# Kernel optimization log

Measured on AMD Instinct MI355X. Metric: run time of the kernel, lower is better.

Reference implementation:

```python
import jax, jax.numpy as jnp
import numpy as np

B, SEQ, DIM = 2, 2048, 1024
HEADS, DIM_HEAD = 16, 64
INNER = HEADS * DIM_HEAD
SCALE = DIM_HEAD ** -0.5


def rotate_half(x):
    # pair consecutive dims (d r) with r=2: (x1, x2) -> (-x2, x1)
    xp = x.reshape(*x.shape[:-1], -1, 2)
    x1, x2 = xp[..., 0], xp[..., 1]
    return jnp.stack((-x2, x1), axis=-1).reshape(x.shape)


def apply_rotary_emb(freqs, t):
    # freqs: [n, rot_dim] angles; t: [b, h, n, d]
    rot_dim = freqs.shape[-1]
    t_rot, t_pass = t[..., :rot_dim], t[..., rot_dim:]
    t_rot = t_rot * jnp.cos(freqs) + rotate_half(t_rot) * jnp.sin(freqs)
    return jnp.concatenate([t_rot, t_pass], axis=-1)


def setup_inputs() -> dict:
    key = jax.random.key(0)
    ks = jax.random.split(key, 4)
    x = jax.random.normal(ks[0], (B, SEQ, DIM), dtype=jnp.float32)
    mask = jnp.ones((B, SEQ), dtype=bool)
    rotary_pos_emb = jax.random.uniform(ks[1], (SEQ, DIM_HEAD), dtype=jnp.float32)
    Wqkv = jax.random.normal(ks[2], (DIM, 3 * INNER), dtype=jnp.float32) * 0.02
    Wout = jax.random.normal(ks[3], (INNER, DIM), dtype=jnp.float32) * 0.02
    bout = jnp.zeros((DIM,), dtype=jnp.float32)
    return {"x": x, "mask": mask, "rotary_pos_emb": rotary_pos_emb,
            "Wqkv": Wqkv, "Wout": Wout, "bout": bout}


def reference(x, mask, rotary_pos_emb, Wqkv, Wout, bout):
    b, n, _ = x.shape
    qkv = x @ Wqkv                                   # [b, n, 3*inner]
    q, k, v = jnp.split(qkv, 3, axis=-1)

    def to_heads(t):
        return t.reshape(b, n, HEADS, DIM_HEAD).transpose(0, 2, 1, 3)  # [b,h,n,d]

    q, k, v = to_heads(q), to_heads(k), to_heads(v)
    freqs = rotary_pos_emb[:n, :]
    # NB: original applies rotary to q, k AND v
    q = apply_rotary_emb(freqs, q)
    k = apply_rotary_emb(freqs, k)
    v = apply_rotary_emb(freqs, v)
    q = q * SCALE

    dots = jnp.einsum('bhid,bhjd->bhij', q, k)       # [b,h,n,n]
    mask_value = -jnp.finfo(dots.dtype).max
    pad = mask[:, None, None, :]                     # [b,1,1,n] keep where True
    dots = jnp.where(pad, dots, mask_value)
    idx = jnp.arange(n)
    causal = idx[None, :] > idx[:, None]             # j >= i + (j-i+1) with i==j==n
    dots = jnp.where(causal[None, None], mask_value, dots)

    attn = jax.nn.softmax(dots, axis=-1)
    out = jnp.einsum('bhij,bhjd->bhid', attn, v)     # [b,h,n,d]
    out = out.transpose(0, 2, 1, 3).reshape(b, n, INNER)
    return out @ Wout + bout
```

## Files before the change

### kernel.cpp

```cpp
#include <hip/hip_runtime.h>
#include <hip/hip_bf16.h>
#include <stdint.h>

#define DEVI __device__ __forceinline__

typedef __bf16 bf16x8 __attribute__((ext_vector_type(8)));
typedef float f32x4 __attribute__((ext_vector_type(4)));
typedef float f32x16 __attribute__((ext_vector_type(16)));

static constexpr int SEQ = 2048;
static constexpr int DIM = 1024;
static constexpr int HEADS = 16;
static constexpr int NQKV = 3072;
static constexpr int MROWS = 4096;
static constexpr float QSCALE = 0.125f;
static constexpr float LOG2E = 1.4426950408889634f;

DEVI unsigned short f2bf(float f) {
  unsigned int u = __builtin_bit_cast(unsigned int, f);
  u += 0x7FFFu + ((u >> 16) & 1u);
  return (unsigned short)(u >> 16);
}

DEVI bf16x8 ld8(const unsigned short* p) {
  return __builtin_bit_cast(bf16x8, *(const uint4*)p);
}

DEVI f32x4 mfma16(bf16x8 a, bf16x8 b, f32x4 c) {
  return __builtin_amdgcn_mfma_f32_16x16x32_bf16(a, b, c, 0, 0, 0);
}

DEVI f32x16 mfma32(bf16x8 a, bf16x8 b, f32x16 c) {
  return __builtin_amdgcn_mfma_f32_32x32x16_bf16(a, b, c, 0, 0, 0);
}

DEVI void load_lds16(const void* g, void* l) {
  __builtin_amdgcn_global_load_lds((const __attribute__((address_space(1))) void*)g,
                                   (__attribute__((address_space(3))) void*)l,
                                   16, 0, 0);
}

DEVI int swz(int row, int kelem) {
  return row * 64 + (kelem ^ ((row & 7) << 3));
}

DEVI unsigned cvtpk(float lo, float hi) {
  unsigned r;
  asm("v_cvt_pk_bf16_f32 %0, %1, %2" : "=v"(r) : "v"(lo), "v"(hi));
  return r;
}

DEVI void pl32swap(unsigned& a, unsigned& b) {
  asm volatile("v_permlane32_swap_b32 %0, %1" : "+v"(a), "+v"(b));
}
DEVI float xhalf_max(float v) { return fmaxf(v, __shfl_xor(v, 32)); }
DEVI float xhalf_sum(float v) { return v + __shfl_xor(v, 32); }

DEVI void transpose_tile(const float* __restrict__ in, unsigned short* __restrict__ out,
                         int Kd, int Nd, int bx, int by, int tid,
                         unsigned short (*T)[68]) {
  const int n0 = bx * 64, k0 = by * 64;
  const int rr = tid >> 4, cc = (tid & 15) * 4;
#pragma unroll
  for (int p = 0; p < 4; ++p) {
    const int r = p * 16 + rr;
    float4 f = *(const float4*)(in + (size_t)(k0 + r) * Nd + n0 + cc);
    T[r][cc + 0] = f2bf(f.x);
    T[r][cc + 1] = f2bf(f.y);
    T[r][cc + 2] = f2bf(f.z);
    T[r][cc + 3] = f2bf(f.w);
  }
  __syncthreads();
#pragma unroll
  for (int p = 0; p < 4; ++p) {
    const int rn = p * 16 + rr;
    ushort4 v;
    v.x = T[cc + 0][rn];
    v.y = T[cc + 1][rn];
    v.z = T[cc + 2][rn];
    v.w = T[cc + 3][rn];
    *(ushort4*)(out + (size_t)(n0 + rn) * Kd + k0 + cc) = v;
  }
}

__global__ __launch_bounds__(256) void k_prep(
    const float* __restrict__ x, unsigned short* __restrict__ xb,
    const float* __restrict__ rope, float* __restrict__ cosb, float* __restrict__ sinb,
    const float* __restrict__ Wqkv, unsigned short* __restrict__ wqkvt,
    const float* __restrict__ Wout, unsigned short* __restrict__ woutt) {
  __shared__ unsigned short T[64][68];
  const int bid = blockIdx.x, tid = threadIdx.x;
  if (bid < 2048) {
    const size_t i = ((size_t)bid * 256 + tid) * 8;
    float4 f0 = *(const float4*)(x + i);
    float4 f1 = *(const float4*)(x + i + 4);
    ushort4 v0, v1;
    v0.x = f2bf(f0.x); v0.y = f2bf(f0.y); v0.z = f2bf(f0.z); v0.w = f2bf(f0.w);
    v1.x = f2bf(f1.x); v1.y = f2bf(f1.y); v1.z = f2bf(f1.z); v1.w = f2bf(f1.w);
    *(ushort4*)(xb + i) = v0;
    *(ushort4*)(xb + i + 4) = v1;
  } else if (bid < 2560) {
    const int i = (bid - 2048) * 256 + tid;
    float f = rope[i];
    cosb[i] = cosf(f);
    sinb[i] = sinf(f);
  } else if (bid < 3328) {
    const int idx = bid - 2560;
    transpose_tile(Wqkv, wqkvt, DIM, NQKV, idx % 48, idx / 48, tid, T);
  } else {
    const int idx = bid - 3328;
    transpose_tile(Wout, woutt, DIM, DIM, idx % 16, idx / 16, tid, T);
  }
}

__global__ __launch_bounds__(512, 1) void k_gemm_qkv(
    const unsigned short* __restrict__ xb, const unsigned short* __restrict__ wt,
    const float* __restrict__ cosb, const float* __restrict__ sinb,
    unsigned short* __restrict__ qb, unsigned short* __restrict__ kb,
    unsigned short* __restrict__ vb) {
  __shared__ __align__(16) unsigned short Ab[2][2][8192];
  __shared__ __align__(16) unsigned short Bb[2][12288];
  const int tid = threadIdx.x, lane = tid & 63, wid = tid >> 6;
  const int wm = wid >> 2, wn = wid & 3;
  const int m0 = blockIdx.x * 256, n0 = blockIdx.y * 192;
  const int la15 = lane & 15, l16 = lane >> 4;
  const int pS0 = tid, pS1 = tid + 512;
  const int sr0 = pS0 >> 3, sr1 = pS1 >> 3;
  const int sc0 = ((pS0 & 7) ^ (sr0 & 7)) * 8, sc1 = ((pS1 & 7) ^ (sr1 & 7)) * 8;
  const int bsr = tid >> 3;
  const int bsc = ((tid & 7) ^ (bsr & 7)) * 8;

  auto stageA = [&](int h, int s) {
    const unsigned short* src = xb + (size_t)(m0 + h * 128) * DIM + s * 64;
    unsigned short* dst = &Ab[s & 1][h][0];
    load_lds16(src + (size_t)sr0 * DIM + sc0, dst + pS0 * 8);
    load_lds16(src + (size_t)sr1 * DIM + sc1, dst + pS1 * 8);
  };
  auto stageB3 = [&](int t, int s) {
    const unsigned short* src = wt + (size_t)(n0 + t * 64 + bsr) * DIM + s * 64;
    load_lds16(src + bsc, &Bb[s & 1][t * 4096] + tid * 8);
  };

  f32x4 acc[8][3] = {};
  stageA(0, 0); stageA(1, 0); stageB3(0, 0); stageB3(1, 0); stageB3(2, 0);
  stageA(0, 1); stageA(1, 1); stageB3(0, 1); stageB3(1, 1); stageB3(2, 1);

#pragma unroll 1
  for (int s = 0; s < 16; ++s) {
    const unsigned short* Ah = &Ab[s & 1][wm][0];
    const unsigned short* Bh = &Bb[s & 1][0];
    const int rb = wn * 48;
    bf16x8 bfr[3][2];
#pragma unroll
    for (int q = 0; q < 4; ++q) {
      if (q == 0) {
        if (s == 0)       asm volatile("s_waitcnt vmcnt(7)" ::: "memory");
        else if (s == 15) asm volatile("s_waitcnt vmcnt(0)" ::: "memory");
        else              asm volatile("s_waitcnt vmcnt(3)" ::: "memory");
        __syncthreads();
      }
      if (q == 2) __syncthreads();
      bf16x8 afr[2][2];
      if (q == 0) {
#pragma unroll
        for (int ni = 0; ni < 3; ++ni)
#pragma unroll
          for (int kk = 0; kk < 2; ++kk)
            bfr[ni][kk] = ld8(&Bh[swz(rb + ni * 16 + la15, kk * 32 + 8 * l16)]);
      }
#pragma unroll
      for (int mi = 0; mi < 2; ++mi)
#pragma unroll
        for (int kk = 0; kk < 2; ++kk)
          afr[mi][kk] = ld8(&Ah[swz(q * 32 + mi * 16 + la15, kk * 32 + 8 * l16)]);
      if (q == 0)      { if (s >= 1 && s + 1 < 16) stageA(0, s + 1); }
      else if (q == 1) { if (s >= 1 && s + 1 < 16) stageA(1, s + 1); }
      else if (q == 2) { if (s + 2 < 16) stageB3(0, s + 2); }
      else             { if (s + 2 < 16) { stageB3(1, s + 2); stageB3(2, s + 2); } }
      asm volatile("s_waitcnt lgkmcnt(0)" ::: "memory");
      __builtin_amdgcn_sched_barrier(0);
      __builtin_amdgcn_s_setprio(1);
#pragma unroll
      for (int kk = 0; kk < 2; ++kk)
#pragma unroll
        for (int mi = 0; mi < 2; ++mi)
#pragma unroll
          for (int ni = 0; ni < 3; ++ni)
            acc[2 * q + mi][ni] = mfma16(afr[mi][kk], bfr[ni][kk], acc[2 * q + mi][ni]);
      __builtin_amdgcn_s_setprio(0);
    }
  }

#pragma unroll
  for (int mq = 0; mq < 8; ++mq) {
#pragma unroll
    for (int ni = 0; ni < 3; ++ni) {
      const int ng = n0 + wn * 48 + ni * 16 + la15;
      const int d = ng & 63;
      const int part = ng >> 10;
      const int h = (ng & 1023) >> 6;
      const int mg0 = m0 + wm * 128 + mq * 16 + 4 * l16;
      const int s0 = mg0 & (SEQ - 1), b = mg0 >> 11;
      const size_t bh = (size_t)(b * HEADS + h);
      if (part == 2) {
        ushort4 vv;
#pragma unroll
        for (int r = 0; r < 4; ++r) {
          const int s = s0 + r;
          float v = acc[mq][ni][r];
          float p = __shfl_xor(v, 1);
          float cv = cosb[(s << 6) + d], sv = sinb[(s << 6) + d];
          float rot = v * cv + ((d & 1) ? p : -p) * sv;
          ((unsigned short*)&vv)[r] = f2bf(rot);
        }
        *(ushort4*)(vb + (bh * 64 + d) * SEQ + s0) = vv;
      } else {
#pragma unroll
        for (int r = 0; r < 4; ++r) {
          const int s = s0 + r;
          float v = acc[mq][ni][r];
          float p = __shfl_xor(v, 1);
          float cv = cosb[(s << 6) + d], sv = sinb[(s << 6) + d];
          float rot = v * cv + ((d & 1) ? p : -p) * sv;
          if (part == 0) {
            qb[(bh * SEQ + s) * 64 + d] = f2bf(rot * (QSCALE * LOG2E));
          } else {
            kb[(bh * SEQ + s) * 64 + d] = f2bf(rot);
          }
        }
      }
    }
  }
}

__global__ __launch_bounds__(256) void k_flash(
    const unsigned short* __restrict__ qb, const unsigned short* __restrict__ kb,
    const unsigned short* __restrict__ vtb, unsigned short* __restrict__ ao) {
  __shared__ __align__(16) unsigned short Ks[2][2][4096];
  __shared__ __align__(16) unsigned short Vt[2][4096];
  const int bh = blockIdx.x;
  const int qt = 31 - blockIdx.y;
  const int tid = threadIdx.x, lane = tid & 63, wid = tid >> 6;
  const int wq = wid >> 1, wk = wid & 1;
  const int la31 = lane & 31, h = lane >> 5;
  const unsigned short* kbh = kb + (size_t)bh * SEQ * 64;
  const unsigned short* vbh = vtb + (size_t)bh * 64 * SEQ;
  const int b = bh >> 4, hh = bh & 15;
  const int sslot = ((lane & 7) ^ (lane >> 3)) * 8;
  float* mrg = (float*)&Ks[0][0][0];
  const int mbase = wq * 2176;

  auto stageK = [&](int buf, int t) {
    const int kv0 = t * 64;
#pragma unroll
    for (int i = 0; i < 4; ++i) {
      const int chunk = wq * 4 + i;
      const int row = chunk * 8 + (lane >> 3);
      load_lds16(kbh + ((size_t)(kv0 + row) << 6) + sslot, &Ks[buf][wk][chunk * 512]);
    }
  };
  auto stageV = [&](int t) {
    const int kv0 = t * 64;
#pragma unroll
    for (int i = 0; i < 4; ++i) {
      const int chunk = wq * 4 + i;
      const int row = chunk * 8 + (lane >> 3);
      load_lds16(vbh + (size_t)row * SEQ + kv0 + sslot, &Vt[wk][chunk * 512]);
    }
  };

  const int q0 = qt * 64 + wq * 32;
  const int qr = q0 + la31;
  const unsigned short* qp = qb + ((size_t)bh * SEQ + qr) * 64;
  bf16x8 qf0 = ld8(qp + 0 + 8 * h);
  bf16x8 qf1 = ld8(qp + 16 + 8 * h);
  bf16x8 qf2 = ld8(qp + 32 + 8 * h);
  bf16x8 qf3 = ld8(qp + 48 + 8 * h);

  f32x16 o0 = {}, o1 = {};
  float m = -1e30f, l = 0.f;
  const int nkv = qt + 1;
  const int nst = (nkv + 1) >> 1;

  if (wk < nkv) stageK(0, wk);
#pragma unroll 1
  for (int st = 0; st < nst; ++st) {
    const int cur = st & 1;
    const int t = 2 * st + wk;
    const bool live = (t < nkv);
    __syncthreads();
    if (live) stageV(t);
    { const int tn = 2 * (st + 1) + wk; if (tn < nkv) stageK(cur ^ 1, tn); }

    bf16x8 pa0, pa1, pa2, pa3;
    if (live) {
      const int kv0 = t * 64;
      const unsigned short* Kc = &Ks[cur][wk][0];
      f32x16 st0 = {}, st1 = {};
      __builtin_amdgcn_s_setprio(1);
#pragma unroll
      for (int ks = 0; ks < 4; ++ks) {
        bf16x8 qk = (ks == 0) ? qf0 : (ks == 1) ? qf1 : (ks == 2) ? qf2 : qf3;
        st0 = mfma32(ld8(&Kc[swz(la31, 16 * ks + 8 * h)]), qk, st0);
        st1 = mfma32(ld8(&Kc[swz(32 + la31, 16 * ks + 8 * h)]), qk, st1);
      }
      __builtin_amdgcn_s_setprio(0);
      if (kv0 + 63 > q0) {
#pragma unroll
        for (int r = 0; r < 16; ++r) {
          const int kvo = (r & 3) + 8 * (r >> 2) + 4 * h;
          st0[r] = (kv0 + kvo > qr) ? -1e30f : st0[r];
          st1[r] = (kv0 + 32 + kvo > qr) ? -1e30f : st1[r];
        }
      }
      float a8[8];
#pragma unroll
      for (int i = 0; i < 8; ++i)
        a8[i] = fmaxf(fmaxf(st0[i], st0[i + 8]), fmaxf(st1[i], st1[i + 8]));
      float a4_0 = fmaxf(a8[0], a8[4]), a4_1 = fmaxf(a8[1], a8[5]);
      float a4_2 = fmaxf(a8[2], a8[6]), a4_3 = fmaxf(a8[3], a8[7]);
      float pmax = fmaxf(fmaxf(a4_0, a4_1), fmaxf(a4_2, a4_3));
      const bool nor = __all(pmax <= m + 8.f);
      float scl = 1.f;
      if (!nor) {
        const float rowmax = xhalf_max(pmax);
        const float mnew = fmaxf(m, rowmax);
        scl = exp2f(m - mnew);
        m = mnew;
      }
#pragma unroll
      for (int r = 0; r < 16; ++r) {
        st0[r] = exp2f(st0[r] - m);
        st1[r] = exp2f(st1[r] - m);
      }
      float s8[8];
#pragma unroll
      for (int i = 0; i < 8; ++i)
        s8[i] = (st0[i] + st0[i + 8]) + (st1[i] + st1[i + 8]);
      float s4_0 = s8[0] + s8[4], s4_1 = s8[1] + s8[5];
      float s4_2 = s8[2] + s8[6], s4_3 = s8[3] + s8[7];
      float psum = (s4_0 + s4_1) + (s4_2 + s4_3);
      const float rowsum = xhalf_sum(psum);
      if (nor) {
        l += rowsum;
      } else {
        l = l * scl + rowsum;
#pragma unroll
        for (int r = 0; r < 16; ++r) { o0[r] *= scl; o1[r] *= scl; }
      }
      unsigned w0 = cvtpk(st0[0], st0[1]),   w1 = cvtpk(st0[2], st0[3]);
      unsigned w2 = cvtpk(st0[4], st0[5]),   w3 = cvtpk(st0[6], st0[7]);
      unsigned w4 = cvtpk(st0[8], st0[9]),   w5 = cvtpk(st0[10], st0[11]);
      unsigned w6 = cvtpk(st0[12], st0[13]), w7 = cvtpk(st0[14], st0[15]);
      pl32swap(w0, w2); pl32swap(w1, w3); pl32swap(w4, w6); pl32swap(w5, w7);
      pa0 = __builtin_bit_cast(bf16x8, (uint4){w0, w1, w2, w3});
      pa1 = __builtin_bit_cast(bf16x8, (uint4){w4, w5, w6, w7});
      unsigned x0 = cvtpk(st1[0], st1[1]),   x1 = cvtpk(st1[2], st1[3]);
      unsigned x2 = cvtpk(st1[4], st1[5]),   x3 = cvtpk(st1[6], st1[7]);
      unsigned x4 = cvtpk(st1[8], st1[9]),   x5 = cvtpk(st1[10], st1[11]);
      unsigned x6 = cvtpk(st1[12], st1[13]), x7 = cvtpk(st1[14], st1[15]);
      pl32swap(x0, x2); pl32swap(x1, x3); pl32swap(x4, x6); pl32swap(x5, x7);
      pa2 = __builtin_bit_cast(bf16x8, (uint4){x0, x1, x2, x3});
      pa3 = __builtin_bit_cast(bf16x8, (uint4){x4, x5, x6, x7});
    }
    __syncthreads();
    if (live) {
      const unsigned short* Vc = &Vt[wk][0];
      __builtin_amdgcn_s_setprio(1);
      o0 = mfma32(ld8(&Vc[swz(la31, 0 + 8 * h)]), pa0, o0);
      o0 = mfma32(ld8(&Vc[swz(la31, 16 + 8 * h)]), pa1, o0);
      o0 = mfma32(ld8(&Vc[swz(la31, 32 + 8 * h)]), pa2, o0);
      o0 = mfma32(ld8(&Vc[swz(la31, 48 + 8 * h)]), pa3, o0);
      o1 = mfma32(ld8(&Vc[swz(32 + la31, 0 + 8 * h)]), pa0, o1);
      o1 = mfma32(ld8(&Vc[swz(32 + la31, 16 + 8 * h)]), pa1, o1);
      o1 = mfma32(ld8(&Vc[swz(32 + la31, 32 + 8 * h)]), pa2, o1);
      o1 = mfma32(ld8(&Vc[swz(32 + la31, 48 + 8 * h)]), pa3, o1);
      __builtin_amdgcn_s_setprio(0);
    }
  }

  __syncthreads();
  if (wk == 1) {
#pragma unroll
    for (int s = 0; s < 8; ++s) {
      f32x4 c;
      if (s < 4) { c[0]=o0[4*s]; c[1]=o0[4*s+1]; c[2]=o0[4*s+2]; c[3]=o0[4*s+3]; }
      else       { c[0]=o1[4*(s-4)]; c[1]=o1[4*(s-4)+1]; c[2]=o1[4*(s-4)+2]; c[3]=o1[4*(s-4)+3]; }
      *(f32x4*)&mrg[mbase + lane * 32 + 4 * (s ^ (lane & 7))] = c;
    }
    mrg[mbase + 2048 + lane] = m;
    mrg[mbase + 2112 + lane] = l;
  }
  __syncthreads();
  if (wk == 0) {
    const float m1 = mrg[mbase + 2048 + lane];
    const float l1 = mrg[mbase + 2112 + lane];
    const float mM = fmaxf(m, m1);
    const float sc0 = exp2f(m - mM), sc1 = exp2f(m1 - mM);
    const float lt = l * sc0 + l1 * sc1;
    const float rl = __builtin_amdgcn_rcpf(lt);
    unsigned short* aor = ao + ((size_t)(b * SEQ + qr)) * 1024 + hh * 64;
#pragma unroll
    for (int s = 0; s < 8; ++s) {
      f32x4 c = *(const f32x4*)&mrg[mbase + lane * 32 + 4 * (s ^ (lane & 7))];
      float v0, v1, v2, v3;
      if (s < 4) {
        v0 = (o0[4*s]   * sc0 + c[0] * sc1) * rl;
        v1 = (o0[4*s+1] * sc0 + c[1] * sc1) * rl;
        v2 = (o0[4*s+2] * sc0 + c[2] * sc1) * rl;
        v3 = (o0[4*s+3] * sc0 + c[3] * sc1) * rl;
      } else {
        v0 = (o1[4*(s-4)]   * sc0 + c[0] * sc1) * rl;
        v1 = (o1[4*(s-4)+1] * sc0 + c[1] * sc1) * rl;
        v2 = (o1[4*(s-4)+2] * sc0 + c[2] * sc1) * rl;
        v3 = (o1[4*(s-4)+3] * sc0 + c[3] * sc1) * rl;
      }
      uint2 uv;
      uv.x = cvtpk(v0, v1);
      uv.y = cvtpk(v2, v3);
      *(uint2*)(aor + (s < 4 ? 8 * s : 32 + 8 * (s - 4)) + 4 * h) = uv;
    }
  }
}

__global__ __launch_bounds__(256) void k_gemm_out(
    const unsigned short* __restrict__ ao, const unsigned short* __restrict__ wt,
    const float* __restrict__ bout, float* __restrict__ out) {
  __shared__ __align__(16) unsigned short As[128 * 64];
  __shared__ __align__(16) unsigned short Bs[64 * 64];
  const int m0 = blockIdx.x * 128, n0 = blockIdx.y * 64;
  const int lane = threadIdx.x & 63, wid = threadIdx.x >> 6;
  const int rsub = lane >> 3;
  const int ksw = ((lane & 7) ^ rsub) * 8;
  f32x4 acc[2][4] = {};
  for (int kt = 0; kt < DIM; kt += 64) {
    __syncthreads();
#pragma unroll
    for (int i = 0; i < 4; ++i) {
      const int chunk = wid * 4 + i;
      const int row = chunk * 8 + rsub;
      load_lds16(ao + (size_t)(m0 + row) * DIM + kt + ksw, As + chunk * 512);
    }
#pragma unroll
    for (int i = 0; i < 2; ++i) {
      const int chunk = wid * 2 + i;
      const int row = chunk * 8 + rsub;
      load_lds16(wt + (size_t)(n0 + row) * DIM + kt + ksw, Bs + chunk * 512);
    }
    __syncthreads();
#pragma unroll
    for (int kk = 0; kk < 2; ++kk) {
      bf16x8 af[2], bfv[4];
#pragma unroll
      for (int mi = 0; mi < 2; ++mi)
        af[mi] = ld8(&As[swz(wid * 32 + mi * 16 + (lane & 15),
                             kk * 32 + 8 * (lane >> 4))]);
#pragma unroll
      for (int ni = 0; ni < 4; ++ni)
        bfv[ni] = ld8(&Bs[swz(ni * 16 + (lane & 15),
                              kk * 32 + 8 * (lane >> 4))]);
#pragma unroll
      for (int mi = 0; mi < 2; ++mi)
#pragma unroll
        for (int ni = 0; ni < 4; ++ni)
          acc[mi][ni] = mfma16(af[mi], bfv[ni], acc[mi][ni]);
    }
  }
#pragma unroll
  for (int mi = 0; mi < 2; ++mi) {
#pragma unroll
    for (int ni = 0; ni < 4; ++ni) {
      const int ng = n0 + ni * 16 + (lane & 15);
      const float bn = bout[ng];
#pragma unroll
      for (int r = 0; r < 4; ++r) {
        const int mg = m0 + wid * 32 + mi * 16 + 4 * (lane >> 4) + r;
        out[(size_t)mg * DIM + ng] = acc[mi][ni][r] + bn;
      }
    }
  }
}

extern "C" void kernel_launch(void* const* d_in, const int* in_sizes, int n_in,
                              void* d_out, int out_size, void* d_ws, size_t ws_size,
                              hipStream_t stream) {
  const float* x    = (const float*)d_in[0];
  const float* rope = (const float*)d_in[2];
  const float* Wqkv = (const float*)d_in[3];
  const float* Wout = (const float*)d_in[4];
  const float* bout = (const float*)d_in[5];
  float* out = (float*)d_out;

  char* ws = (char*)d_ws;
  unsigned short* xb    = (unsigned short*)(ws + 0);
  unsigned short* wqkvt = (unsigned short*)(ws + 8388608);
  unsigned short* woutt = (unsigned short*)(ws + 14680064);
  float*          cosb  = (float*)(ws + 16777216);
  float*          sinb  = (float*)(ws + 17301504);
  unsigned short* qbuf  = (unsigned short*)(ws + 17825792);
  unsigned short* kbuf  = (unsigned short*)(ws + 26214400);
  unsigned short* vbuf  = (unsigned short*)(ws + 34603008);
  unsigned short* aob   = (unsigned short*)(ws + 42991616);

  k_prep<<<3584, 256, 0, stream>>>(x, xb, rope, cosb, sinb, Wqkv, wqkvt, Wout, woutt);
  k_gemm_qkv<<<dim3(16, 16), 512, 0, stream>>>(xb, wqkvt, cosb, sinb,
                                               qbuf, kbuf, vbuf);
  k_flash<<<dim3(32, 32), 256, 0, stream>>>(qbuf, kbuf, vbuf, aob);
  k_gemm_out<<<dim3(32, 16), 256, 0, stream>>>(aob, woutt, bout, out);
}
```

Before: 114.9 us.

## Pair causal query tiles per block and split KV across four waves

The flash kernel now launches half as many blocks with 512 threads. Each block processes two query tiles (31-j and j) so causal work is balanced across blocks. KV is split into 32-row sub-tiles spread over four waves per query group, with a two-stage tree merge of the partial softmax states through LDS. This targets tail imbalance and raises per-block parallelism, at the cost of extra barriers and merge traffic.

```diff
diff --git a/kernel.cpp b/kernel.cpp
--- a/kernel.cpp
+++ b/kernel.cpp
@@ -233,193 +233,216 @@
   }
 }
 
-__global__ __launch_bounds__(256) void k_flash(
+__global__ __launch_bounds__(512, 4) void k_flash(
     const unsigned short* __restrict__ qb, const unsigned short* __restrict__ kb,
     const unsigned short* __restrict__ vtb, unsigned short* __restrict__ ao) {
-  __shared__ __align__(16) unsigned short Ks[2][2][4096];
-  __shared__ __align__(16) unsigned short Vt[2][4096];
+  __shared__ __align__(16) unsigned short LDS[24576];
+  unsigned short (*Ks)[4][2048] = (unsigned short (*)[4][2048])&LDS[0];
+  unsigned short (*Vt)[2048] = (unsigned short (*)[2048])&LDS[16384];
+  float* scr = (float*)&LDS[0];
   const int bh = blockIdx.x;
-  const int qt = 31 - blockIdx.y;
+  const int j = blockIdx.y;
   const int tid = threadIdx.x, lane = tid & 63, wid = tid >> 6;
-  const int wq = wid >> 1, wk = wid & 1;
+  const int wq = wid >> 2, wk = wid & 3;
   const int la31 = lane & 31, h = lane >> 5;
   const unsigned short* kbh = kb + (size_t)bh * SEQ * 64;
   const unsigned short* vbh = vtb + (size_t)bh * 64 * SEQ;
   const int b = bh >> 4, hh = bh & 15;
-  const int sslot = ((lane & 7) ^ (lane >> 3)) * 8;
-  float* mrg = (float*)&Ks[0][0][0];
-  const int mbase = wq * 2176;
+
+  const int pA = wq * 128 + lane, pB = pA + 64;
+  const int rA = pA >> 3, rB = pB >> 3;
+  const int cA = (pA & 7) ^ (rA & 7), cB = (pB & 7) ^ (rB & 7);
+  const int kconA = rA * 64 + cA * 8, kconB = rB * 64 + cB * 8;
+  const int vconA = (2 * rA + (cA >> 2)) * SEQ + (cA & 3) * 8;
+  const int vconB = (2 * rB + (cB >> 2)) * SEQ + (cB & 3) * 8;
 
   auto stageK = [&](int buf, int t) {
-    const int kv0 = t * 64;
-#pragma unroll
-    for (int i = 0; i < 4; ++i) {
-      const int chunk = wq * 4 + i;
-      const int row = chunk * 8 + (lane >> 3);
-      load_lds16(kbh + ((size_t)(kv0 + row) << 6) + sslot, &Ks[buf][wk][chunk * 512]);
-    }
+    const size_t kv0 = (size_t)t * 32;
+    unsigned short* Kd = &Ks[buf][wk][0];
+    load_lds16(kbh + kv0 * 64 + kconA, Kd + pA * 8);
+    load_lds16(kbh + kv0 * 64 + kconB, Kd + pB * 8);
   };
   auto stageV = [&](int t) {
-    const int kv0 = t * 64;
-#pragma unroll
-    for (int i = 0; i < 4; ++i) {
-      const int chunk = wq * 4 + i;
-      const int row = chunk * 8 + (lane >> 3);
-      load_lds16(vbh + (size_t)row * SEQ + kv0 + sslot, &Vt[wk][chunk * 512]);
-    }
+    const size_t kv0 = (size_t)t * 32;
+    unsigned short* Vd = &Vt[wk][0];
+    load_lds16(vbh + kv0 + vconA, Vd + pA * 8);
+    load_lds16(vbh + kv0 + vconB, Vd + pB * 8);
   };
 
-  const int q0 = qt * 64 + wq * 32;
-  const int qr = q0 + la31;
-  const unsigned short* qp = qb + ((size_t)bh * SEQ + qr) * 64;
-  bf16x8 qf0 = ld8(qp + 0 + 8 * h);
-  bf16x8 qf1 = ld8(qp + 16 + 8 * h);
-  bf16x8 qf2 = ld8(qp + 32 + 8 * h);
-  bf16x8 qf3 = ld8(qp + 48 + 8 * h);
-
-  f32x16 o0 = {}, o1 = {};
-  float m = -1e30f, l = 0.f;
-  const int nkv = qt + 1;
-  const int nst = (nkv + 1) >> 1;
-
-  if (wk < nkv) stageK(0, wk);
 #pragma unroll 1
-  for (int st = 0; st < nst; ++st) {
-    const int cur = st & 1;
-    const int t = 2 * st + wk;
-    const bool live = (t < nkv);
-    __syncthreads();
-    if (live) stageV(t);
-    { const int tn = 2 * (st + 1) + wk; if (tn < nkv) stageK(cur ^ 1, tn); }
-
-    bf16x8 pa0, pa1, pa2, pa3;
-    if (live) {
-      const int kv0 = t * 64;
-      const unsigned short* Kc = &Ks[cur][wk][0];
-      f32x16 st0 = {}, st1 = {};
-      __builtin_amdgcn_s_setprio(1);
-#pragma unroll
-      for (int ks = 0; ks < 4; ++ks) {
-        bf16x8 qk = (ks == 0) ? qf0 : (ks == 1) ? qf1 : (ks == 2) ? qf2 : qf3;
-        st0 = mfma32(ld8(&Kc[swz(la31, 16 * ks + 8 * h)]), qk, st0);
-        st1 = mfma32(ld8(&Kc[swz(32 + la31, 16 * ks + 8 * h)]), qk, st1);
-      }
-      __builtin_amdgcn_s_setprio(0);
-      if (kv0 + 63 > q0) {
-#pragma unroll
-        for (int r = 0; r < 16; ++r) {
-          const int kvo = (r & 3) + 8 * (r >> 2) + 4 * h;
-          st0[r] = (kv0 + kvo > qr) ? -1e30f : st0[r];
-          st1[r] = (kv0 + 32 + kvo > qr) ? -1e30f : st1[r];
-        }
-      }
-      float a8[8];
-#pragma unroll
-      for (int i = 0; i < 8; ++i)
-        a8[i] = fmaxf(fmaxf(st0[i], st0[i + 8]), fmaxf(st1[i], st1[i + 8]));
-      float a4_0 = fmaxf(a8[0], a8[4]), a4_1 = fmaxf(a8[1], a8[5]);
-      float a4_2 = fmaxf(a8[2], a8[6]), a4_3 = fmaxf(a8[3], a8[7]);
-      float pmax = fmaxf(fmaxf(a4_0, a4_1), fmaxf(a4_2, a4_3));
-      const bool nor = __all(pmax <= m + 8.f);
-      float scl = 1.f;
-      if (!nor) {
-        const float rowmax = xhalf_max(pmax);
-        const float mnew = fmaxf(m, rowmax);
-        scl = exp2f(m - mnew);
-        m = mnew;
-      }
-#pragma unroll
-      for (int r = 0; r < 16; ++r) {
-        st0[r] = exp2f(st0[r] - m);
-        st1[r] = exp2f(st1[r] - m);
-      }
-      float s8[8];
-#pragma unroll
-      for (int i = 0; i < 8; ++i)
-        s8[i] = (st0[i] + st0[i + 8]) + (st1[i] + st1[i + 8]);
-      float s4_0 = s8[0] + s8[4], s4_1 = s8[1] + s8[5];
-      float s4_2 = s8[2] + s8[6], s4_3 = s8[3] + s8[7];
-      float psum = (s4_0 + s4_1) + (s4_2 + s4_3);
-      const float rowsum = xhalf_sum(psum);
-      if (nor) {
-        l += rowsum;
-      } else {
-        l = l * scl + rowsum;
-#pragma unroll
-        for (int r = 0; r < 16; ++r) { o0[r] *= scl; o1[r] *= scl; }
-      }
-      unsigned w0 = cvtpk(st0[0], st0[1]),   w1 = cvtpk(st0[2], st0[3]);
-      unsigned w2 = cvtpk(st0[4], st0[5]),   w3 = cvtpk(st0[6], st0[7]);
-      unsigned w4 = cvtpk(st0[8], st0[9]),   w5 = cvtpk(st0[10], st0[11]);
-      unsigned w6 = cvtpk(st0[12], st0[13]), w7 = cvtpk(st0[14], st0[15]);
-      pl32swap(w0, w2); pl32swap(w1, w3); pl32swap(w4, w6); pl32swap(w5, w7);
-      pa0 = __builtin_bit_cast(bf16x8, (uint4){w0, w1, w2, w3});
-      pa1 = __builtin_bit_cast(bf16x8, (uint4){w4, w5, w6, w7});
-      unsigned x0 = cvtpk(st1[0], st1[1]),   x1 = cvtpk(st1[2], st1[3]);
-      unsigned x2 = cvtpk(st1[4], st1[5]),   x3 = cvtpk(st1[6], st1[7]);
-      unsigned x4 = cvtpk(st1[8], st1[9]),   x5 = cvtpk(st1[10], st1[11]);
-      unsigned x6 = cvtpk(st1[12], st1[13]), x7 = cvtpk(st1[14], st1[15]);
-      pl32swap(x0, x2); pl32swap(x1, x3); pl32swap(x4, x6); pl32swap(x5, x7);
-      pa2 = __builtin_bit_cast(bf16x8, (uint4){x0, x1, x2, x3});
-      pa3 = __builtin_bit_cast(bf16x8, (uint4){x4, x5, x6, x7});
-    }
-    __syncthreads();
-    if (live) {
-      const unsigned short* Vc = &Vt[wk][0];
-      __builtin_amdgcn_s_setprio(1);
-      o0 = mfma32(ld8(&Vc[swz(la31, 0 + 8 * h)]), pa0, o0);
-      o0 = mfma32(ld8(&Vc[swz(la31, 16 + 8 * h)]), pa1, o0);
-      o0 = mfma32(ld8(&Vc[swz(la31, 32 + 8 * h)]), pa2, o0);
-      o0 = mfma32(ld8(&Vc[swz(la31, 48 + 8 * h)]), pa3, o0);
-      o1 = mfma32(ld8(&Vc[swz(32 + la31, 0 + 8 * h)]), pa0, o1);
-      o1 = mfma32(ld8(&Vc[swz(32 + la31, 16 + 8 * h)]), pa1, o1);
-      o1 = mfma32(ld8(&Vc[swz(32 + la31, 32 + 8 * h)]), pa2, o1);
-      o1 = mfma32(ld8(&Vc[swz(32 + la31, 48 + 8 * h)]), pa3, o1);
-      __builtin_amdgcn_s_setprio(0);
-    }
-  }
-
-  __syncthreads();
-  if (wk == 1) {
-#pragma unroll
-    for (int s = 0; s < 8; ++s) {
-      f32x4 c;
-      if (s < 4) { c[0]=o0[4*s]; c[1]=o0[4*s+1]; c[2]=o0[4*s+2]; c[3]=o0[4*s+3]; }
-      else       { c[0]=o1[4*(s-4)]; c[1]=o1[4*(s-4)+1]; c[2]=o1[4*(s-4)+2]; c[3]=o1[4*(s-4)+3]; }
-      *(f32x4*)&mrg[mbase + lane * 32 + 4 * (s ^ (lane & 7))] = c;
-    }
-    mrg[mbase + 2048 + lane] = m;
-    mrg[mbase + 2112 + lane] = l;
-  }
-  __syncthreads();
-  if (wk == 0) {
-    const float m1 = mrg[mbase + 2048 + lane];
-    const float l1 = mrg[mbase + 2112 + lane];
-    const float mM = fmaxf(m, m1);
-    const float sc0 = exp2f(m - mM), sc1 = exp2f(m1 - mM);
-    const float lt = l * sc0 + l1 * sc1;
-    const float rl = __builtin_amdgcn_rcpf(lt);
-    unsigned short* aor = ao + ((size_t)(b * SEQ + qr)) * 1024 + hh * 64;
-#pragma unroll
-    for (int s = 0; s < 8; ++s) {
-      f32x4 c = *(const f32x4*)&mrg[mbase + lane * 32 + 4 * (s ^ (lane & 7))];
-      float v0, v1, v2, v3;
-      if (s < 4) {
-        v0 = (o0[4*s]   * sc0 + c[0] * sc1) * rl;
-        v1 = (o0[4*s+1] * sc0 + c[1] * sc1) * rl;
-        v2 = (o0[4*s+2] * sc0 + c[2] * sc1) * rl;
-        v3 = (o0[4*s+3] * sc0 + c[3] * sc1) * rl;
-      } else {
-        v0 = (o1[4*(s-4)]   * sc0 + c[0] * sc1) * rl;
-        v1 = (o1[4*(s-4)+1] * sc0 + c[1] * sc1) * rl;
-        v2 = (o1[4*(s-4)+2] * sc0 + c[2] * sc1) * rl;
-        v3 = (o1[4*(s-4)+3] * sc0 + c[3] * sc1) * rl;
-      }
-      uint2 uv;
-      uv.x = cvtpk(v0, v1);
-      uv.y = cvtpk(v2, v3);
-      *(uint2*)(aor + (s < 4 ? 8 * s : 32 + 8 * (s - 4)) + 4 * h) = uv;
-    }
+  for (int hf = 0; hf < 2; ++hf) {
+    const int qt = hf == 0 ? (31 - j) : j;
+    const int q0 = qt * 64 + wq * 32;
+    const int qr = q0 + la31;
+    const unsigned short* qp = qb + ((size_t)bh * SEQ + qr) * 64;
+    bf16x8 qf0 = ld8(qp + 0 + 8 * h);
+    bf16x8 qf1 = ld8(qp + 16 + 8 * h);
+    bf16x8 qf2 = ld8(qp + 32 + 8 * h);
+    bf16x8 qf3 = ld8(qp + 48 + 8 * h);
+
+    f32x16 o0 = {}, o1 = {};
+    float m = -1e30f, l = 0.f;
+    const int nkv = 2 * qt + 2;
+    const int nlay = (nkv + 3) >> 2;
+
+    if (wk < nkv) stageK(0, wk);
+#pragma unroll 1
+    for (int L = 0; L < nlay; ++L) {
+      const int buf = L & 1;
+      const int t = 4 * L + wk;
+      const bool exists = (t < nkv);
+      const bool live = exists && (t * 32 <= q0 + 31);
+      __syncthreads();
+      if (exists) stageV(t);
+      { const int tn = 4 * (L + 1) + wk; if (tn < nkv) stageK(buf ^ 1, tn); }
+
+      bf16x8 pa0, pa1;
+      f32x16 st = {};
+      if (live) {
+        const int kv0 = t * 32;
+        const unsigned short* Kc = &Ks[buf][wk][0];
+        __builtin_amdgcn_s_setprio(1);
+        st = mfma32(ld8(&Kc[swz(la31, 0 + 8 * h)]), qf0, st);
+        st = mfma32(ld8(&Kc[swz(la31, 16 + 8 * h)]), qf1, st);
+        st = mfma32(ld8(&Kc[swz(la31, 32 + 8 * h)]), qf2, st);
+        st = mfma32(ld8(&Kc[swz(la31, 48 + 8 * h)]), qf3, st);
+        __builtin_amdgcn_s_setprio(0);
+        if (kv0 + 31 > q0) {
+#pragma unroll
+          for (int r = 0; r < 16; ++r) {
+            const int kvo = (r & 3) + 8 * (r >> 2) + 4 * h;
+            st[r] = (kv0 + kvo > qr) ? -1e30f : st[r];
+          }
+        }
+        float a8[8];
+#pragma unroll
+        for (int i = 0; i < 8; ++i) a8[i] = fmaxf(st[i], st[i + 8]);
+        float a4_0 = fmaxf(a8[0], a8[4]), a4_1 = fmaxf(a8[1], a8[5]);
+        float a4_2 = fmaxf(a8[2], a8[6]), a4_3 = fmaxf(a8[3], a8[7]);
+        float pmax = fmaxf(fmaxf(a4_0, a4_1), fmaxf(a4_2, a4_3));
+        const bool nor = __all(pmax <= m + 8.f);
+        float scl = 1.f;
+        if (!nor) {
+          const float rowmax = xhalf_max(pmax);
+          const float mnew = fmaxf(m, rowmax);
+          scl = exp2f(m - mnew);
+          m = mnew;
+        }
+#pragma unroll
+        for (int r = 0; r < 16; ++r) st[r] = exp2f(st[r] - m);
+        float s8[8];
+#pragma unroll
+        for (int i = 0; i < 8; ++i) s8[i] = st[i] + st[i + 8];
+        float s4_0 = s8[0] + s8[4], s4_1 = s8[1] + s8[5];
+        float s4_2 = s8[2] + s8[6], s4_3 = s8[3] + s8[7];
+        float psum = (s4_0 + s4_1) + (s4_2 + s4_3);
+        const float rowsum = xhalf_sum(psum);
+        if (nor) {
+          l += rowsum;
+        } else {
+          l = l * scl + rowsum;
+#pragma unroll
+          for (int r = 0; r < 16; ++r) { o0[r] *= scl; o1[r] *= scl; }
+        }
+        unsigned w0 = cvtpk(st[0], st[1]),   w1 = cvtpk(st[2], st[3]);
+        unsigned w2 = cvtpk(st[4], st[5]),   w3 = cvtpk(st[6], st[7]);
+        unsigned w4 = cvtpk(st[8], st[9]),   w5 = cvtpk(st[10], st[11]);
+        unsigned w6 = cvtpk(st[12], st[13]), w7 = cvtpk(st[14], st[15]);
+        pl32swap(w0, w2); pl32swap(w1, w3); pl32swap(w4, w6); pl32swap(w5, w7);
+        pa0 = __builtin_bit_cast(bf16x8, (uint4){w0, w1, w2, w3});
+        pa1 = __builtin_bit_cast(bf16x8, (uint4){w4, w5, w6, w7});
+      }
+      __syncthreads();
+      if (live) {
+        const unsigned short* Vc = &Vt[wk][0];
+        const int rv = la31 >> 1;
+        const int cb = 32 * (la31 & 1) + 8 * h;
+        __builtin_amdgcn_s_setprio(1);
+        o0 = mfma32(ld8(&Vc[swz(rv, cb)]), pa0, o0);
+        o0 = mfma32(ld8(&Vc[swz(rv, cb + 16)]), pa1, o0);
+        o1 = mfma32(ld8(&Vc[swz(16 + rv, cb)]), pa0, o1);
+        o1 = mfma32(ld8(&Vc[swz(16 + rv, cb + 16)]), pa1, o1);
+        __builtin_amdgcn_s_setprio(0);
+      }
+    }
+
+    __syncthreads();
+    if (wk >= 2) {
+      float* rg = scr + (wq * 2 + (wk - 2)) * 2176;
+#pragma unroll
+      for (int s = 0; s < 8; ++s) {
+        f32x4 c;
+        if (s < 4) { c[0]=o0[4*s]; c[1]=o0[4*s+1]; c[2]=o0[4*s+2]; c[3]=o0[4*s+3]; }
+        else { c[0]=o1[4*(s-4)]; c[1]=o1[4*(s-4)+1]; c[2]=o1[4*(s-4)+2]; c[3]=o1[4*(s-4)+3]; }
+        *(f32x4*)&rg[lane * 32 + 4 * (s ^ (lane & 7))] = c;
+      }
+      rg[2048 + lane] = m;
+      rg[2112 + lane] = l;
+    }
+    __syncthreads();
+    if (wk < 2) {
+      float* rg = scr + (wq * 2 + wk) * 2176;
+      const float m1 = rg[2048 + lane], l1 = rg[2112 + lane];
+      const float mM = fmaxf(m, m1);
+      const float sc0 = exp2f(m - mM), sc1 = exp2f(m1 - mM);
+      m = mM;
+      l = l * sc0 + l1 * sc1;
+#pragma unroll
+      for (int s = 0; s < 8; ++s) {
+        f32x4 c = *(const f32x4*)&rg[lane * 32 + 4 * (s ^ (lane & 7))];
+        if (s < 4) {
+#pragma unroll
+          for (int q = 0; q < 4; ++q) o0[4*s+q] = o0[4*s+q] * sc0 + c[q] * sc1;
+        } else {
+#pragma unroll
+          for (int q = 0; q < 4; ++q) o1[4*(s-4)+q] = o1[4*(s-4)+q] * sc0 + c[q] * sc1;
+        }
+      }
+    }
+    __syncthreads();
+    if (wk == 1) {
+      float* rg = scr + (wq * 2) * 2176;
+#pragma unroll
+      for (int s = 0; s < 8; ++s) {
+        f32x4 c;
+        if (s < 4) { c[0]=o0[4*s]; c[1]=o0[4*s+1]; c[2]=o0[4*s+2]; c[3]=o0[4*s+3]; }
+        else { c[0]=o1[4*(s-4)]; c[1]=o1[4*(s-4)+1]; c[2]=o1[4*(s-4)+2]; c[3]=o1[4*(s-4)+3]; }
+        *(f32x4*)&rg[lane * 32 + 4 * (s ^ (lane & 7))] = c;
+      }
+      rg[2048 + lane] = m;
+      rg[2112 + lane] = l;
+    }
+    __syncthreads();
+    if (wk == 0) {
+      float* rg = scr + (wq * 2) * 2176;
+      const float m1 = rg[2048 + lane], l1 = rg[2112 + lane];
+      const float mM = fmaxf(m, m1);
+      const float sc0 = exp2f(m - mM), sc1 = exp2f(m1 - mM);
+      const float lt = l * sc0 + l1 * sc1;
+      const float rl = __builtin_amdgcn_rcpf(lt);
+      unsigned short* aor = ao + ((size_t)(b * SEQ + qr)) * 1024 + hh * 64;
+#pragma unroll
+      for (int s = 0; s < 8; ++s) {
+        f32x4 c = *(const f32x4*)&rg[lane * 32 + 4 * (s ^ (lane & 7))];
+        float v0, v1, v2, v3;
+        if (s < 4) {
+          v0 = (o0[4*s]   * sc0 + c[0] * sc1) * rl;
+          v1 = (o0[4*s+1] * sc0 + c[1] * sc1) * rl;
+          v2 = (o0[4*s+2] * sc0 + c[2] * sc1) * rl;
+          v3 = (o0[4*s+3] * sc0 + c[3] * sc1) * rl;
+        } else {
+          v0 = (o1[4*(s-4)]   * sc0 + c[0] * sc1) * rl;
+          v1 = (o1[4*(s-4)+1] * sc0 + c[1] * sc1) * rl;
+          v2 = (o1[4*(s-4)+2] * sc0 + c[2] * sc1) * rl;
+          v3 = (o1[4*(s-4)+3] * sc0 + c[3] * sc1) * rl;
+        }
+        uint2 uv;
+        uv.x = cvtpk(v0, v1);
+        uv.y = cvtpk(v2, v3);
+        *(uint2*)(aor + (s < 4 ? 8 * s : 32 + 8 * (s - 4)) + 4 * h) = uv;
+      }
+    }
+    __syncthreads();
   }
 }
 
@@ -505,6 +528,6 @@
   k_prep<<<3584, 256, 0, stream>>>(x, xb, rope, cosb, sinb, Wqkv, wqkvt, Wout, woutt);
   k_gemm_qkv<<<dim3(16, 16), 512, 0, stream>>>(xb, wqkvt, cosb, sinb,
                                                qbuf, kbuf, vbuf);
-  k_flash<<<dim3(32, 32), 256, 0, stream>>>(qbuf, kbuf, vbuf, aob);
+  k_flash<<<dim3(32, 16), 512, 0, stream>>>(qbuf, kbuf, vbuf, aob);
   k_gemm_out<<<dim3(32, 16), 256, 0, stream>>>(aob, woutt, bout, out);
 }
```

Result: no change. 116.4 us (+1.3%).
